# Kernel tuning notes

Hardware: AMD Instinct MI355X
Metric: run time of the kernel (lower is better)

Reference implementation:

```python
import jax, jax.numpy as jnp
import numpy as np

B, S, D = 2, 2048, 2048
HQ, HKV = 32, 8
DH = D // HQ  # 64
NUM_REP = HQ // HKV  # 4


def setup_inputs() -> dict:
    key = jax.random.key(0)
    k1, k2, k3, k4, k5 = jax.random.split(key, 5)
    scale = 0.02
    return {
        "x": jax.random.normal(k1, (B, S, D), dtype=jnp.float32),
        "Wq": jax.random.normal(k2, (D, HQ * DH), dtype=jnp.float32) * scale,
        "Wk": jax.random.normal(k3, (D, HKV * DH), dtype=jnp.float32) * scale,
        "Wv": jax.random.normal(k4, (D, HKV * DH), dtype=jnp.float32) * scale,
        "Wo": jax.random.normal(k5, (HQ * DH, D), dtype=jnp.float32) * scale,
    }


def reference(x, Wq, Wk, Wv, Wo):
    b, s, _ = x.shape
    # projections
    xq = (x @ Wq).reshape(b, s, HQ, DH)    # [B,S,HQ,DH]
    xk = (x @ Wk).reshape(b, s, HKV, DH)   # [B,S,HKV,DH]
    xv = (x @ Wv).reshape(b, s, HKV, DH)
    # repeat kv heads to match query heads (GQA expand)
    keys = jnp.repeat(xk, NUM_REP, axis=2)    # [B,S,HQ,DH]
    values = jnp.repeat(xv, NUM_REP, axis=2)
    # scores: [B,HQ,S,S], fp32 softmax (no causal mask in original)
    scores = jnp.einsum("bqhd,bkhd->bhqk", xq, keys) / jnp.sqrt(jnp.float32(DH))
    probs = jax.nn.softmax(scores.astype(jnp.float32), axis=-1).astype(xq.dtype)
    context = jnp.einsum("bhqk,bkhd->bqhd", probs, values)  # [B,S,HQ,DH]
    context = context.reshape(b, s, HQ * DH)
    return context @ Wo
```

## Files before the change

### kernel.cpp

```cpp
#include <hip/hip_runtime.h>
#include <cstdint>
#include <cstddef>
#include <cmath>

typedef __bf16 bf16x8 __attribute__((ext_vector_type(8)));
typedef float  f32x4  __attribute__((ext_vector_type(4)));
typedef unsigned short us4 __attribute__((ext_vector_type(4)));

__device__ __forceinline__ unsigned short f2bf(float f) {
    union { float f; unsigned int u; } v; v.f = f;
    unsigned int u = v.u;
    u += 0x7fffu + ((u >> 16) & 1u);
    return (unsigned short)(u >> 16);
}

__device__ __forceinline__ unsigned int fbits(float f) {
    union { float f; unsigned int u; } v; v.f = f; return v.u;
}

__device__ __forceinline__ unsigned int pk_bf16_trunc(float a, float b) {
    return __builtin_amdgcn_perm(fbits(b), fbits(a), 0x07060302u);
}

__device__ __forceinline__ void gld_lds16(const void* g, void* l) {
    __builtin_amdgcn_global_load_lds((__attribute__((address_space(1))) void*)g,
                                     (__attribute__((address_space(3))) void*)l,
                                     16, 0, 0);
}

#define BB   2
#define SS   2048
#define DD   2048
#define HQ   32
#define HKV  8
#define DH   64
#define MM   (BB * SS)
#define NQKV 3072

#define QSCALE 0.18033688011112042f

__global__ __launch_bounds__(256) void prep(const float* __restrict__ x,
                                            const float* __restrict__ Wq,
                                            const float* __restrict__ Wk,
                                            const float* __restrict__ Wv,
                                            const float* __restrict__ Wo,
                                            unsigned short* __restrict__ xb,
                                            unsigned short* __restrict__ WqkvT,
                                            unsigned short* __restrict__ WoT) {
    const int bid = blockIdx.x;
    if (bid < 8192) {
        const int i = (bid * 256 + threadIdx.x) * 4;
        const float4 f = *(const float4*)(x + i);
        us4 o;
        o[0] = f2bf(f.x); o[1] = f2bf(f.y); o[2] = f2bf(f.z); o[3] = f2bf(f.w);
        *(us4*)(xb + i) = o;
        return;
    }
    const float* src; unsigned short* dst; int C, bx, by; float scl = 1.0f;
    int r = bid - 8192;
    if (r < 4096) {
        src = Wq; dst = WqkvT; C = 2048; bx = r & 63; by = r >> 6; scl = QSCALE;
    } else if (r < 8192) {
        r -= 4096; src = Wo; dst = WoT; C = 2048; bx = r & 63; by = r >> 6;
    } else if (r < 9216) {
        r -= 8192; src = Wk; dst = WqkvT + (size_t)2048 * 2048; C = 512; bx = r & 15; by = r >> 4;
    } else {
        r -= 9216; src = Wv; dst = WqkvT + (size_t)2560 * 2048; C = 512; bx = r & 15; by = r >> 4;
    }
    const int R = 2048;
    __shared__ __attribute__((aligned(16))) float tile[32][33];
    const int c0 = bx * 32, r0 = by * 32;
    const int tx = threadIdx.x & 31, ty = threadIdx.x >> 5;
    #pragma unroll
    for (int dy = 0; dy < 32; dy += 8)
        tile[ty + dy][tx] = src[(size_t)(r0 + ty + dy) * C + c0 + tx];
    __syncthreads();
    #pragma unroll
    for (int dy = 0; dy < 32; dy += 8)
        dst[(size_t)(c0 + ty + dy) * R + r0 + tx] = f2bf(tile[tx][ty + dy] * scl);
}

__global__ __launch_bounds__(256) void transpose_v(const unsigned short* __restrict__ qkv,
                                                   unsigned short* __restrict__ vt) {
    __shared__ __attribute__((aligned(16))) unsigned short tile[32][33];
    const int s0 = blockIdx.x * 32, d0 = blockIdx.y * 32;
    const int bh = blockIdx.z;
    const int b = bh >> 3, kvh = bh & 7;
    const int tx = threadIdx.x & 31, ty = threadIdx.x >> 5;
    #pragma unroll
    for (int dy = 0; dy < 32; dy += 8)
        tile[ty + dy][tx] =
            qkv[(size_t)(b * SS + s0 + ty + dy) * NQKV + 2560 + kvh * DH + d0 + tx];
    __syncthreads();
    #pragma unroll
    for (int dy = 0; dy < 32; dy += 8)
        vt[(size_t)((b * HKV + kvh) * DH + d0 + ty + dy) * SS + s0 + tx] =
            tile[tx][ty + dy];
}

template <int OUT_BF16>
__global__ __launch_bounds__(256) void gemm_bt(const unsigned short* __restrict__ A,
                                               const unsigned short* __restrict__ Bt,
                                               void* __restrict__ Cout,
                                               int M, int N, int K) {
    __shared__ __attribute__((aligned(16))) unsigned short As[128 * 64];
    __shared__ __attribute__((aligned(16))) unsigned short Bs[128 * 64];
    const int bm = blockIdx.x, bn = blockIdx.y;
    const int tid = threadIdx.x;
    const int wave = tid >> 6, lane = tid & 63;
    const int wm = (wave >> 1) * 64, wn = (wave & 1) * 64;
    const int g = lane >> 4, l15 = lane & 15;
    const int sr = lane >> 3;
    const int sc8 = ((lane & 7) ^ (sr & 7)) * 8;
    const int r7 = l15 & 7;

    f32x4 acc[4][4] = {};
    const unsigned short* aBase = A  + (size_t)(bm * 128) * K;
    const unsigned short* bBase = Bt + (size_t)(bn * 128) * K;

    for (int kt = 0; kt < K; kt += 64) {
        __syncthreads();
        #pragma unroll
        for (int j = 0; j < 4; ++j) {
            const int i = wave * 4 + j;
            gld_lds16(aBase + (size_t)(i * 8 + sr) * K + kt + sc8, &As[i * 512]);
            gld_lds16(bBase + (size_t)(i * 8 + sr) * K + kt + sc8, &Bs[i * 512]);
        }
        __syncthreads();
        #pragma unroll
        for (int ks = 0; ks < 2; ++ks) {
            bf16x8 af[4], bfr[4];
            #pragma unroll
            for (int t = 0; t < 4; ++t) {
                af[t]  = *(const bf16x8*)&As[(wm + t * 16 + l15) * 64 + ((ks * 4 + g) ^ r7) * 8];
                bfr[t] = *(const bf16x8*)&Bs[(wn + t * 16 + l15) * 64 + ((ks * 4 + g) ^ r7) * 8];
            }
            #pragma unroll
            for (int i = 0; i < 4; ++i)
                #pragma unroll
                for (int j = 0; j < 4; ++j)
                    acc[i][j] = __builtin_amdgcn_mfma_f32_16x16x32_bf16(
                        af[i], bfr[j], acc[i][j], 0, 0, 0);
        }
    }
    #pragma unroll
    for (int i = 0; i < 4; ++i) {
        #pragma unroll
        for (int j = 0; j < 4; ++j) {
            const int col = bn * 128 + wn + j * 16 + l15;
            #pragma unroll
            for (int r = 0; r < 4; ++r) {
                const int row = bm * 128 + wm + i * 16 + g * 4 + r;
                const float v = acc[i][j][r];
                if (OUT_BF16)
                    ((unsigned short*)Cout)[(size_t)row * N + col] = f2bf(v);
                else
                    ((float*)Cout)[(size_t)row * N + col] = v;
            }
        }
    }
}

__global__ __launch_bounds__(256, 4) void flash_attn(const unsigned short* __restrict__ qkv,
                                                     const unsigned short* __restrict__ vt,
                                                     unsigned short* __restrict__ ctx) {
    __shared__ __attribute__((aligned(16))) unsigned short Ks[2][64 * 64];
    __shared__ __attribute__((aligned(16))) unsigned short Vs[2][64 * 64];

    const int qt = blockIdx.x, h = blockIdx.y, b = blockIdx.z;
    const int kvh = h >> 2;
    const int tid = threadIdx.x, wave = tid >> 6, lane = tid & 63;
    const int g = lane >> 4, l15 = lane & 15;
    const int sr = lane >> 3;
    const int sc8 = ((lane & 7) ^ (sr & 7)) * 8;
    const int r7 = l15 & 7;
    const int qb = qt * 128 + wave * 32;

    const unsigned short* kbase = qkv + (size_t)(b * SS) * NQKV + 2048 + kvh * DH;
    const unsigned short* vbase = vt + (size_t)((b * HKV + kvh) * DH) * SS;

    bf16x8 qf[2][2];
    #pragma unroll
    for (int n = 0; n < 2; ++n)
        #pragma unroll
        for (int kh = 0; kh < 2; ++kh)
            qf[n][kh] = *(const bf16x8*)(qkv +
                (size_t)(b * SS + qb + n * 16 + l15) * NQKV + h * DH + kh * 32 + g * 8);

    bf16x8 ones;
    #pragma unroll
    for (int i = 0; i < 8; ++i) ones[i] = (__bf16)1.0f;

    const f32x4 z4 = {0.0f, 0.0f, 0.0f, 0.0f};

    const unsigned short* sp[4];
    size_t sadv;
    if (wave < 2) {
        #pragma unroll
        for (int j = 0; j < 4; ++j) {
            const int rho = (wave * 4 + j) * 8 + sr;
            const int key = (rho & 0x23) | ((rho & 0x0C) << 1) | ((rho & 0x10) >> 2);
            sp[j] = kbase + (size_t)key * NQKV + sc8;
        }
        sadv = (size_t)64 * NQKV;
    } else {
        #pragma unroll
        for (int j = 0; j < 4; ++j)
            sp[j] = vbase + (size_t)(((wave - 2) * 4 + j) * 8 + sr) * SS + sc8;
        sadv = 64;
    }

    #define STAGE(buf)                                                        \
        do {                                                                  \
            if (wave < 2) {                                                   \
                _Pragma("unroll")                                             \
                for (int j = 0; j < 4; ++j)                                   \
                    gld_lds16(sp[j], &Ks[buf][(wave * 4 + j) * 512]);         \
            } else {                                                          \
                _Pragma("unroll")                                             \
                for (int j = 0; j < 4; ++j)                                   \
                    gld_lds16(sp[j], &Vs[buf][((wave - 2) * 4 + j) * 512]);   \
            }                                                                 \
            _Pragma("unroll")                                                 \
            for (int j = 0; j < 4; ++j) sp[j] += sadv;                        \
        } while (0)

    f32x4 oacc[2][4] = {};
    f32x4 lacc[2] = {};

    #define TILE(BUF)                                                                          \
        do {                                                                                   \
            const unsigned short* ks = Ks[BUF];                                                \
            const unsigned short* vs = Vs[BUF];                                                \
            _Pragma("unroll")                                                                  \
            for (int p = 0; p < 2; ++p) {                                                      \
                uint4 pk4[2];                                                                  \
                _Pragma("unroll")                                                              \
                for (int hh = 0; hh < 2; ++hh) {                                               \
                    const int t = 2 * p + hh;                                                  \
                    bf16x8 kf0 = *(const bf16x8*)&ks[(t * 16 + l15) * 64 + ((g) ^ r7) * 8];    \
                    bf16x8 kf1 = *(const bf16x8*)&ks[(t * 16 + l15) * 64 + ((4 + g) ^ r7) * 8];\
                    _Pragma("unroll")                                                          \
                    for (int n = 0; n < 2; ++n) {                                              \
                        f32x4 c = __builtin_amdgcn_mfma_f32_16x16x32_bf16(                     \
                            kf0, qf[n][0], z4, 0, 0, 0);                                       \
                        c = __builtin_amdgcn_mfma_f32_16x16x32_bf16(                           \
                            kf1, qf[n][1], c, 0, 0, 0);                                        \
                        f32x4 pe;                                                              \
                        pe[0] = __builtin_amdgcn_exp2f(c[0]);                                  \
                        pe[1] = __builtin_amdgcn_exp2f(c[1]);                                  \
                        pe[2] = __builtin_amdgcn_exp2f(c[2]);                                  \
                        pe[3] = __builtin_amdgcn_exp2f(c[3]);                                  \
                        const unsigned int lo = pk_bf16_trunc(pe[0], pe[1]);                   \
                        const unsigned int hi = pk_bf16_trunc(pe[2], pe[3]);                   \
                        if (hh == 0) { pk4[n].x = lo; pk4[n].y = hi; }                         \
                        else         { pk4[n].z = lo; pk4[n].w = hi; }                         \
                    }                                                                          \
                }                                                                              \
                __builtin_amdgcn_s_setprio(1);                                                 \
                _Pragma("unroll")                                                              \
                for (int nt = 0; nt < 4; ++nt) {                                               \
                    bf16x8 vf = *(const bf16x8*)&vs[(nt * 16 + l15) * 64 +                     \
                                                    (((p << 2) + g) ^ r7) * 8];                \
                    _Pragma("unroll")                                                          \
                    for (int m = 0; m < 2; ++m) {                                              \
                        union { uint4 u; bf16x8 v; } pa; pa.u = pk4[m];                        \
                        oacc[m][nt] = __builtin_amdgcn_mfma_f32_16x16x32_bf16(                 \
                            pa.v, vf, oacc[m][nt], 0, 0, 0);                                   \
                        if (nt == 0)                                                           \
                            lacc[m] = __builtin_amdgcn_mfma_f32_16x16x32_bf16(                 \
                                pa.v, ones, lacc[m], 0, 0, 0);                                 \
                    }                                                                          \
                }                                                                              \
                __builtin_amdgcn_s_setprio(0);                                                 \
            }                                                                                  \
        } while (0)

    STAGE(0);

    #pragma unroll 1
    for (int kt2 = 0; kt2 < 16; ++kt2) {
        __syncthreads();
        STAGE(1);
        TILE(0);
        __syncthreads();
        if (kt2 < 15) STAGE(0);
        TILE(1);
    }

    #pragma unroll
    for (int m = 0; m < 2; ++m) {
        #pragma unroll
        for (int r = 0; r < 4; ++r) {
            const float inv = __builtin_amdgcn_rcpf(lacc[m][r]);
            const int token = b * SS + qb + m * 16 + g * 4 + r;
            #pragma unroll
            for (int nt = 0; nt < 4; ++nt)
                ctx[(size_t)token * (HQ * DH) + h * DH + nt * 16 + l15] =
                    f2bf(oacc[m][nt][r] * inv);
        }
    }
    #undef TILE
    #undef STAGE
}

extern "C" void kernel_launch(void* const* d_in, const int* in_sizes, int n_in,
                              void* d_out, int out_size, void* d_ws, size_t ws_size,
                              hipStream_t stream) {
    (void)in_sizes; (void)n_in; (void)out_size; (void)ws_size;
    const float* x  = (const float*)d_in[0];
    const float* Wq = (const float*)d_in[1];
    const float* Wk = (const float*)d_in[2];
    const float* Wv = (const float*)d_in[3];
    const float* Wo = (const float*)d_in[4];
    float* out = (float*)d_out;

    char* ws = (char*)d_ws;
    unsigned short* xb     = (unsigned short*)(ws);
    unsigned short* WqkvT  = (unsigned short*)(ws + 16777216);
    unsigned short* WoT    = (unsigned short*)(ws + 29360128);
    unsigned short* QKV    = (unsigned short*)(ws + 37748736);
    unsigned short* Vt     = (unsigned short*)(ws + 62914560);
    unsigned short* ctx    = (unsigned short*)(ws + 67108864);

    prep<<<18432, 256, 0, stream>>>(x, Wq, Wk, Wv, Wo, xb, WqkvT, WoT);

    gemm_bt<1><<<dim3(32, 24), 256, 0, stream>>>(xb, WqkvT, QKV, MM, NQKV, DD);

    transpose_v<<<dim3(64, 2, 16), 256, 0, stream>>>(QKV, Vt);

    flash_attn<<<dim3(16, 32, 2), 256, 0, stream>>>(QKV, Vt, ctx);

    gemm_bt<0><<<dim3(32, 16), 256, 0, stream>>>(ctx, WoT, out, MM, DD, DD);
}
```

Before: 287.2 us.

## Add double-buffered 256x256 GEMM for QKV projection and swizzle block order

Replaces the QKV projection GEMM with a new 512-thread kernel that uses 256x256 tiles, double-buffered LDS staging via direct global-to-LDS loads, explicit vmcnt waits and s_setprio around the MFMA bursts. The output GEMM keeps its 128x128 kernel but takes a 1D grid with remapped block indices so neighbouring blocks share A/B tiles in L2. The goals are more data reuse per tile, overlap of loads with MFMA work, and better L2 locality. The larger tile uses 128KB of LDS and yields only 192 blocks, which may underfill the 256 CUs, and the K-loop count is hardcoded to 16 iterations, which assumes K=2048.

```diff
diff --git a/kernel.cpp b/kernel.cpp
--- a/kernel.cpp
+++ b/kernel.cpp
@@ -98,14 +98,130 @@
             tile[tx][ty + dy];
 }
 
+__global__ __launch_bounds__(512, 2) void gemm256(const unsigned short* __restrict__ A,
+                                                  const unsigned short* __restrict__ Bt,
+                                                  unsigned short* __restrict__ Cout,
+                                                  int M, int N, int K) {
+    __shared__ __attribute__((aligned(16))) unsigned short As[2][256 * 64];
+    __shared__ __attribute__((aligned(16))) unsigned short Bs[2][256 * 64];
+    const int lid = blockIdx.x;
+    const int bm = ((lid & 7) << 1) | ((lid >> 3) & 1);
+    const int bn = lid >> 4;
+    const int tid = threadIdx.x;
+    const int wv = tid >> 6, lane = tid & 63;
+    const int wm = (wv >> 2) * 128;
+    const int wn = (wv & 3) * 64;
+    const int g = lane >> 4, l15 = lane & 15;
+    const int sr = lane >> 3;
+    const int sc8 = ((lane & 7) ^ (sr & 7)) * 8;
+    const int r7 = l15 & 7;
+
+    f32x4 acc[8][4] = {};
+    const unsigned short* spA[4];
+    const unsigned short* spB[4];
+    #pragma unroll
+    for (int j = 0; j < 4; ++j) {
+        const int row = (wv * 4 + j) * 8 + sr;
+        spA[j] = A  + (size_t)(bm * 256 + row) * K + sc8;
+        spB[j] = Bt + (size_t)(bn * 256 + row) * K + sc8;
+    }
+
+    #define GSTAGE(BUF)                                                       \
+        do {                                                                  \
+            _Pragma("unroll")                                                 \
+            for (int j = 0; j < 4; ++j) {                                     \
+                gld_lds16(spA[j], &As[BUF][(wv * 4 + j) * 512]);              \
+                gld_lds16(spB[j], &Bs[BUF][(wv * 4 + j) * 512]);              \
+                spA[j] += 64; spB[j] += 64;                                   \
+            }                                                                 \
+        } while (0)
+
+    #define GCOMPUTE(BUF)                                                     \
+        do {                                                                  \
+            const unsigned short* as = As[BUF];                               \
+            const unsigned short* bs = Bs[BUF];                               \
+            bf16x8 bfr[4][2];                                                 \
+            _Pragma("unroll")                                                 \
+            for (int n = 0; n < 4; ++n)                                       \
+                _Pragma("unroll")                                             \
+                for (int ks = 0; ks < 2; ++ks)                                \
+                    bfr[n][ks] = *(const bf16x8*)&bs[(wn + n * 16 + l15) * 64 \
+                                                 + ((ks * 4 + g) ^ r7) * 8];  \
+            _Pragma("unroll")                                                 \
+            for (int q = 0; q < 4; ++q) {                                     \
+                bf16x8 af[2][2];                                              \
+                _Pragma("unroll")                                             \
+                for (int mi = 0; mi < 2; ++mi)                                \
+                    _Pragma("unroll")                                         \
+                    for (int ks = 0; ks < 2; ++ks)                            \
+                        af[mi][ks] = *(const bf16x8*)&as[                     \
+                            (wm + (q * 2 + mi) * 16 + l15) * 64               \
+                            + ((ks * 4 + g) ^ r7) * 8];                       \
+                __builtin_amdgcn_s_setprio(1);                                \
+                _Pragma("unroll")                                             \
+                for (int ks = 0; ks < 2; ++ks)                                \
+                    _Pragma("unroll")                                         \
+                    for (int mi = 0; mi < 2; ++mi)                            \
+                        _Pragma("unroll")                                     \
+                        for (int n = 0; n < 4; ++n)                           \
+                            acc[q * 2 + mi][n] =                              \
+                                __builtin_amdgcn_mfma_f32_16x16x32_bf16(      \
+                                    af[mi][ks], bfr[n][ks],                   \
+                                    acc[q * 2 + mi][n], 0, 0, 0);             \
+                __builtin_amdgcn_s_setprio(0);                                \
+            }                                                                 \
+        } while (0)
+
+    GSTAGE(0);
+    GSTAGE(1);
+    asm volatile("s_waitcnt vmcnt(8)" ::: "memory");
+    __builtin_amdgcn_s_barrier();
+
+    #pragma unroll 1
+    for (int t2 = 0; t2 < 16; ++t2) {
+        GCOMPUTE(0);
+        __builtin_amdgcn_s_barrier();
+        if (t2 < 15) {
+            GSTAGE(0);
+            asm volatile("s_waitcnt vmcnt(8)" ::: "memory");
+        } else {
+            asm volatile("s_waitcnt vmcnt(0)" ::: "memory");
+        }
+        __builtin_amdgcn_s_barrier();
+        GCOMPUTE(1);
+        if (t2 == 15) break;
+        __builtin_amdgcn_s_barrier();
+        GSTAGE(1);
+        asm volatile("s_waitcnt vmcnt(8)" ::: "memory");
+        __builtin_amdgcn_s_barrier();
+    }
+
+    #pragma unroll
+    for (int i = 0; i < 8; ++i) {
+        #pragma unroll
+        for (int n = 0; n < 4; ++n) {
+            const int col = bn * 256 + wn + n * 16 + l15;
+            #pragma unroll
+            for (int r = 0; r < 4; ++r) {
+                const int row = bm * 256 + wm + i * 16 + g * 4 + r;
+                Cout[(size_t)row * N + col] = f2bf(acc[i][n][r]);
+            }
+        }
+    }
+    #undef GSTAGE
+    #undef GCOMPUTE
+}
+
 template <int OUT_BF16>
 __global__ __launch_bounds__(256) void gemm_bt(const unsigned short* __restrict__ A,
                                                const unsigned short* __restrict__ Bt,
                                                void* __restrict__ Cout,
-                                               int M, int N, int K) {
+                                               int M, int N, int K, int mbits) {
     __shared__ __attribute__((aligned(16))) unsigned short As[128 * 64];
     __shared__ __attribute__((aligned(16))) unsigned short Bs[128 * 64];
-    const int bm = blockIdx.x, bn = blockIdx.y;
+    const int lid = blockIdx.x;
+    const int bm = ((lid & 7) << mbits) | ((lid >> 3) & ((1 << mbits) - 1));
+    const int bn = lid >> (3 + mbits);
     const int tid = threadIdx.x;
     const int wave = tid >> 6, lane = tid & 63;
     const int wm = (wave >> 1) * 64, wn = (wave & 1) * 64;
@@ -325,11 +441,11 @@
 
     prep<<<18432, 256, 0, stream>>>(x, Wq, Wk, Wv, Wo, xb, WqkvT, WoT);
 
-    gemm_bt<1><<<dim3(32, 24), 256, 0, stream>>>(xb, WqkvT, QKV, MM, NQKV, DD);
+    gemm256<<<192, 512, 0, stream>>>(xb, WqkvT, QKV, MM, NQKV, DD);
 
     transpose_v<<<dim3(64, 2, 16), 256, 0, stream>>>(QKV, Vt);
 
     flash_attn<<<dim3(16, 32, 2), 256, 0, stream>>>(QKV, Vt, ctx);
 
-    gemm_bt<0><<<dim3(32, 16), 256, 0, stream>>>(ctx, WoT, out, MM, DD, DD);
-}
+    gemm_bt<0><<<512, 256, 0, stream>>>(ctx, WoT, out, MM, DD, DD, 2);
+}
```

After: 297.3 us. 1.04x slower.
